# Kernel tuning notes

Measured on AMD Instinct MI355X. Metric: run time of the kernel, lower is better.

## Reference

```python
import jax, jax.numpy as jnp
import numpy as np

D = 512; N = 4096; NH = 16; DEPTH = 3; MLP = 4; GENES = 250; GH = 64; GW = 64


def setup_inputs() -> dict:
    key = jax.random.key(0)
    ks = jax.random.split(key, 10)
    gf = jax.random.normal(ks[0], (N, D), jnp.float32)
    # unique spot positions: permutation of the 64x64 grid cells
    perm = jax.random.permutation(ks[1], GH * GW)[:N]
    coords = jnp.stack([perm // GW, perm % GW], axis=1).astype(jnp.int32)
    s = 0.02
    rn = lambda k, sh: jax.random.normal(k, sh, jnp.float32) * s
    return dict(
        global_feats=gf, coords=coords, grid_h=GH, grid_w=GW,
        ln1_g=jnp.ones((DEPTH, D)), ln1_b=jnp.zeros((DEPTH, D)),
        wqkv=rn(ks[2], (DEPTH, 3 * D, D)), bqkv=jnp.zeros((DEPTH, 3 * D)),
        wo=rn(ks[3], (DEPTH, D, D)), bo=jnp.zeros((DEPTH, D)),
        ln2_g=jnp.ones((DEPTH, D)), ln2_b=jnp.zeros((DEPTH, D)),
        w1=rn(ks[4], (DEPTH, MLP * D, D)), b1=jnp.zeros((DEPTH, MLP * D)),
        w2=rn(ks[5], (DEPTH, D, MLP * D)), b2=jnp.zeros((DEPTH, D)),
        ck=rn(ks[6], (DEPTH, D, 1, 3, 3)), cb=jnp.zeros((DEPTH, D)),
        lnf_g=jnp.ones((D,)), lnf_b=jnp.zeros((D,)),
        wp=rn(ks[7], (GENES, D)), bp=jnp.zeros((GENES,)),
    )


def _ln(x, g, b, eps=1e-5):
    m = jnp.mean(x, axis=-1, keepdims=True)
    v = jnp.var(x, axis=-1, keepdims=True)
    return (x - m) * jax.lax.rsqrt(v + eps) * g + b


def reference(global_feats, coords, grid_h, grid_w, ln1_g, ln1_b, wqkv, bqkv,
              wo, bo, ln2_g, ln2_b, w1, b1, w2, b2, ck, cb, lnf_g, lnf_b, wp, bp):
    x = global_feats  # [N, D]
    n, d = x.shape
    nh = NH; dh = d // nh
    rows = coords[:, 0]; cols = coords[:, 1]
    for i in range(ln1_g.shape[0]):
        # --- self-attention (eval mode, dropout off) ---
        xn = _ln(x, ln1_g[i], ln1_b[i])
        qkv = xn @ wqkv[i].T + bqkv[i]                      # [N, 3D]
        q, k, v = jnp.split(qkv, 3, axis=-1)
        q = q.reshape(n, nh, dh).transpose(1, 0, 2)        # [H, N, dh]
        k = k.reshape(n, nh, dh).transpose(1, 0, 2)
        v = v.reshape(n, nh, dh).transpose(1, 0, 2)
        att = jax.nn.softmax(jnp.einsum('hqd,hkd->hqk', q, k) * (dh ** -0.5), axis=-1)
        ao = jnp.einsum('hqk,hkd->hqd', att, v).transpose(1, 0, 2).reshape(n, d)
        x = x + (ao @ wo[i].T + bo[i])
        # --- MLP ---
        h = jax.nn.gelu(_ln(x, ln2_g[i], ln2_b[i]) @ w1[i].T + b1[i], approximate=False)
        x = x + (h @ w2[i].T + b2[i])
        # --- APEG: scatter -> depthwise conv -> gather ---
        grid = jnp.zeros((d, grid_h, grid_w), x.dtype).at[:, rows, cols].set(x.T)
        co = jax.lax.conv_general_dilated(
            grid[None], ck[i], window_strides=(1, 1), padding=((1, 1), (1, 1)),
            dimension_numbers=('NCHW', 'OIHW', 'NCHW'), feature_group_count=d)[0]
        co = co + cb[i][:, None, None]
        x = x + co[:, rows, cols].T
    x = _ln(x, lnf_g, lnf_b)
    pred = x @ wp.T + bp
    return (x, pred)
```

## Files before the change

kernel.cpp:

```cpp
#include <hip/hip_runtime.h>
#include <math.h>

#define D 512
#define N_TOK 4096
#define NHEAD 16
#define DH 32
#define DEPTH 3
#define MLPD 2048
#define GENES 250
#define GH 64
#define GW 64

typedef __attribute__((ext_vector_type(8))) short short8;
typedef __attribute__((ext_vector_type(4))) float f32x4;
typedef unsigned short ushort_t;

#define AS1 __attribute__((address_space(1)))
#define AS3 __attribute__((address_space(3)))

#if defined(__has_builtin)
#if __has_builtin(__builtin_amdgcn_exp2f)
#define EXP2F(x) __builtin_amdgcn_exp2f(x)
#endif
#endif
#ifndef EXP2F
#define EXP2F(x) __expf(0.69314718056f * (x))
#endif

__device__ __forceinline__ unsigned short f2bf(float f) {
  unsigned int u = __float_as_uint(f);
  u += 0x7fffu + ((u >> 16) & 1u);
  return (unsigned short)(u >> 16);
}
__device__ __forceinline__ unsigned int bfpack(float a, float b) {
  return __builtin_amdgcn_perm(__float_as_uint(b), __float_as_uint(a), 0x07060302u);
}
__device__ __forceinline__ void gload_lds16(const ushort_t* g, ushort_t* l) {
  __builtin_amdgcn_global_load_lds(
      (const AS1 unsigned int*)g,
      (AS3 unsigned int*)(unsigned int)(unsigned long long)l, 16, 0, 0);
}
__device__ __forceinline__ int perm64(int m) {
  int mi = m >> 4, g = (m >> 2) & 3, r = m & 3;
  return ((mi & 1) << 5) | (g << 3) | ((mi >> 1) << 2) | r;
}

__global__ __launch_bounds__(256) void ln_kernel(const float* __restrict__ x,
    const float* __restrict__ g, const float* __restrict__ b,
    float* __restrict__ yf, ushort_t* __restrict__ ybf) {
  int row = blockIdx.x;
  int t = threadIdx.x;
  const float* xr = x + (size_t)row * D;
  float v0 = xr[t], v1 = xr[t + 256];
  float s = v0 + v1;
  float sq = v0 * v0 + v1 * v1;
#pragma unroll
  for (int off = 32; off > 0; off >>= 1) {
    s += __shfl_down(s, off, 64);
    sq += __shfl_down(sq, off, 64);
  }
  __shared__ float s1[4], s2[4];
  int wid = t >> 6, lane = t & 63;
  if (lane == 0) { s1[wid] = s; s2[wid] = sq; }
  __syncthreads();
  float tot = s1[0] + s1[1] + s1[2] + s1[3];
  float totq = s2[0] + s2[1] + s2[2] + s2[3];
  float mean = tot * (1.0f / D);
  float var = totq * (1.0f / D) - mean * mean;
  float rs = rsqrtf(var + 1e-5f);
  float r0 = (v0 - mean) * rs * g[t] + b[t];
  float r1 = (v1 - mean) * rs * g[t + 256] + b[t + 256];
  if (yf) { yf[(size_t)row * D + t] = r0; yf[(size_t)row * D + t + 256] = r1; }
  if (ybf) {
    ybf[(size_t)row * D + t] = f2bf(r0);
    ybf[(size_t)row * D + t + 256] = f2bf(r1);
  }
}

template <int TM, int TN, int NKH>
__global__ __launch_bounds__(256) void gemm_bf(
    const ushort_t* __restrict__ A, const ushort_t* __restrict__ B,
    const float* __restrict__ bias, const float* __restrict__ res,
    float* __restrict__ C, ushort_t* __restrict__ Cbf,
    ushort_t* __restrict__ qO, ushort_t* __restrict__ kO, ushort_t* __restrict__ vO,
    int K, int ldc, int nstore, int mode) {
  constexpr int MI = TM / 32;
  constexpr int NI = TN / 32;
  __shared__ ushort_t As[2][NKH][TM * 32];
  __shared__ ushort_t Bs[2][NKH][TN * 32];
  int t = threadIdx.x;
  int w = t >> 6, lane = t & 63;
  int g = lane >> 4, c = lane & 15;
  int bm = blockIdx.y * TM, bn = blockIdx.x * TN;
  int wr = (w >> 1) * (TM / 2);
  int wc = (w & 1) * (TN / 2);

  const ushort_t* gA = A + (size_t)(bm + (t >> 2)) * K + (t & 3) * 8;
  const ushort_t* gB = B + (size_t)(bn + (t >> 2)) * K + (t & 3) * 8;

  auto stage = [&](int p, int koff) {
#pragma unroll
    for (int h = 0; h < NKH; ++h) {
      gload_lds16(gA + koff + h * 32, &As[p][h][t * 8]);
      if (TM == 128)
        gload_lds16(gA + koff + h * 32 + (size_t)64 * K, &As[p][h][(t + 256) * 8]);
      gload_lds16(gB + koff + h * 32, &Bs[p][h][t * 8]);
      if (TN == 128)
        gload_lds16(gB + koff + h * 32 + (size_t)64 * K, &Bs[p][h][(t + 256) * 8]);
    }
  };

  f32x4 acc[MI][NI] = {};

  const int niter = K / (32 * NKH);
  stage(0, 0);
  __syncthreads();
  for (int it = 0; it < niter; ++it) {
    int p = it & 1;
    if (it + 1 < niter) stage(p ^ 1, (it + 1) * 32 * NKH);
#pragma unroll
    for (int kh = 0; kh < NKH; ++kh) {
      short8 af[MI], bfr[NI];
#pragma unroll
      for (int mi = 0; mi < MI; ++mi)
        af[mi] = *(const short8*)&As[p][kh][(wr + mi * 16 + c) * 32 + g * 8];
#pragma unroll
      for (int ni = 0; ni < NI; ++ni)
        bfr[ni] = *(const short8*)&Bs[p][kh][(wc + ni * 16 + c) * 32 + g * 8];
#pragma unroll
      for (int mi = 0; mi < MI; ++mi)
#pragma unroll
        for (int ni = 0; ni < NI; ++ni)
          acc[mi][ni] = __builtin_amdgcn_mfma_f32_16x16x32_bf16(
              af[mi], bfr[ni], acc[mi][ni], 0, 0, 0);
    }
    __syncthreads();
  }

  const float qs_scale = 0.17677669529663688f * 1.4426950408889634f;
  if (mode == 2) {
#pragma unroll
    for (int ni = 0; ni < NI; ++ni) {
      int col = bn + wc + ni * 16 + c;
      float bv = bias[col];
      int which = col >> 9;
      int h = (col >> 5) & 15;
      int d = col & 31;
      size_t hb = (size_t)h * (N_TOK * DH);
#pragma unroll
      for (int mi = 0; mi < MI; ++mi) {
        int row0 = bm + wr + mi * 16 + g * 4;
        float v0 = acc[mi][ni][0] + bv;
        float v1 = acc[mi][ni][1] + bv;
        float v2 = acc[mi][ni][2] + bv;
        float v3 = acc[mi][ni][3] + bv;
        if (which == 0) {
          qO[hb + (size_t)(row0 + 0) * DH + d] = f2bf(v0 * qs_scale);
          qO[hb + (size_t)(row0 + 1) * DH + d] = f2bf(v1 * qs_scale);
          qO[hb + (size_t)(row0 + 2) * DH + d] = f2bf(v2 * qs_scale);
          qO[hb + (size_t)(row0 + 3) * DH + d] = f2bf(v3 * qs_scale);
        } else if (which == 1) {
          kO[hb + (size_t)(row0 + 0) * DH + d] = f2bf(v0);
          kO[hb + (size_t)(row0 + 1) * DH + d] = f2bf(v1);
          kO[hb + (size_t)(row0 + 2) * DH + d] = f2bf(v2);
          kO[hb + (size_t)(row0 + 3) * DH + d] = f2bf(v3);
        } else {
          int m = row0 & 63;
          int mi_l = m >> 4, g_l = (m >> 2) & 3;
          int nb = ((mi_l & 1) << 5) | (g_l << 3) | ((mi_l >> 1) << 2);
          uint2 pk;
          pk.x = (unsigned)f2bf(v0) | ((unsigned)f2bf(v1) << 16);
          pk.y = (unsigned)f2bf(v2) | ((unsigned)f2bf(v3) << 16);
          *(uint2*)(vO + hb + (size_t)d * N_TOK + (row0 & ~63) + nb) = pk;
        }
      }
    }
    return;
  }
#pragma unroll
  for (int ni = 0; ni < NI; ++ni) {
    int col = bn + wc + ni * 16 + c;
    float bv = bias[col];
    bool cok = col < nstore;
#pragma unroll
    for (int mi = 0; mi < MI; ++mi) {
      int row0 = bm + wr + mi * 16 + g * 4;
#pragma unroll
      for (int reg = 0; reg < 4; ++reg) {
        int row = row0 + reg;
        float v = acc[mi][ni][reg] + bv;
        if (mode == 0) {
          size_t idx = (size_t)row * ldc + col;
          if (cok) {
            if (res) v += res[idx];
            C[idx] = v;
          }
        } else {
          v = 0.5f * v * (1.0f + erff(v * 0.70710678118654752f));
          Cbf[(size_t)row * ldc + col] = f2bf(v);
        }
      }
    }
  }
}

#define VTST 72

__global__ __launch_bounds__(256) void attn_mfma(
    const ushort_t* __restrict__ qb, const ushort_t* __restrict__ kb,
    const ushort_t* __restrict__ vtb, ushort_t* __restrict__ ao) {
  __shared__ ushort_t Vts[2][32 * VTST];
  int qt = blockIdx.x, head = blockIdx.y;
  int t = threadIdx.x;
  int w = t >> 6, lane = t & 63;
  int g = lane >> 4, c = lane & 15;
  const size_t hbase = (size_t)head * (N_TOK * DH);
  int q0 = qt * 128 + w * 32;

  short8 qf[2];
  qf[0] = *(const short8*)(qb + hbase + (size_t)(q0 + c) * DH + g * 8);
  qf[1] = *(const short8*)(qb + hbase + (size_t)(q0 + 16 + c) * DH + g * 8);

  short8 ones;
#pragma unroll
  for (int i = 0; i < 8; ++i) ones[i] = (short)0x3F80;

  f32x4 o[2][2] = {};
  f32x4 lf[2] = {};
  const f32x4 zf = {0.f, 0.f, 0.f, 0.f};

  const ushort_t* vg = vtb + hbase + (size_t)(t >> 3) * N_TOK + (t & 7) * 8;
  const int vofs = (t >> 3) * VTST + (t & 7) * 8;
  const ushort_t* kp = kb + hbase + (size_t)c * DH + g * 8;

  constexpr int NT = N_TOK / 64;
  typedef union { short8 s8; unsigned int u32[4]; } pk_t;

  short8 kfb[2][4];
#pragma unroll
  for (int mi = 0; mi < 4; ++mi)
    kfb[0][mi] = *(const short8*)(kp + (size_t)(mi * 16) * DH);
  {
    short8 v0 = *(const short8*)vg;
    *(short8*)&Vts[0][vofs] = v0;
  }
  short8 vreg = *(const short8*)(vg + 64);
  __syncthreads();

#pragma unroll 2
  for (int tile = 0; tile < NT; ++tile) {
    const int p = tile & 1;
    if (tile + 1 < NT) {
      *(short8*)&Vts[p ^ 1][vofs] = vreg;
      if (tile + 2 < NT) vreg = *(const short8*)(vg + (size_t)(tile + 2) * 64);
#pragma unroll
      for (int mi = 0; mi < 4; ++mi)
        kfb[p ^ 1][mi] =
            *(const short8*)(kp + (size_t)((tile + 1) * 64 + mi * 16) * DH);
    }

    short8 vf[2][2];
#pragma unroll
    for (int half = 0; half < 2; ++half)
#pragma unroll
      for (int ch = 0; ch < 2; ++ch)
        vf[half][ch] = *(const short8*)&Vts[p][(half * 16 + c) * VTST + ch * 32 + g * 8];

    short8 pf[2][2];
#pragma unroll
    for (int qs = 0; qs < 2; ++qs) {
      f32x4 sp[4];
      __builtin_amdgcn_s_setprio(1);
#pragma unroll
      for (int mi = 0; mi < 4; ++mi)
        sp[mi] = __builtin_amdgcn_mfma_f32_16x16x32_bf16(kfb[p][mi], qf[qs], zf, 0, 0, 0);
      __builtin_amdgcn_s_setprio(0);
      float pr[4][4];
#pragma unroll
      for (int mi = 0; mi < 4; ++mi)
#pragma unroll
        for (int r = 0; r < 4; ++r) pr[mi][r] = EXP2F(sp[mi][r]);
      pk_t p0, p1;
      p0.u32[0] = bfpack(pr[0][0], pr[0][1]);
      p0.u32[1] = bfpack(pr[0][2], pr[0][3]);
      p0.u32[2] = bfpack(pr[2][0], pr[2][1]);
      p0.u32[3] = bfpack(pr[2][2], pr[2][3]);
      p1.u32[0] = bfpack(pr[1][0], pr[1][1]);
      p1.u32[1] = bfpack(pr[1][2], pr[1][3]);
      p1.u32[2] = bfpack(pr[3][0], pr[3][1]);
      p1.u32[3] = bfpack(pr[3][2], pr[3][3]);
      pf[qs][0] = p0.s8;
      pf[qs][1] = p1.s8;
    }

    __builtin_amdgcn_s_setprio(1);
#pragma unroll
    for (int qs = 0; qs < 2; ++qs) {
#pragma unroll
      for (int ch = 0; ch < 2; ++ch) {
        lf[qs] = __builtin_amdgcn_mfma_f32_16x16x32_bf16(ones, pf[qs][ch], lf[qs], 0, 0, 0);
#pragma unroll
        for (int half = 0; half < 2; ++half)
          o[qs][half] = __builtin_amdgcn_mfma_f32_16x16x32_bf16(
              vf[half][ch], pf[qs][ch], o[qs][half], 0, 0, 0);
      }
    }
    __builtin_amdgcn_s_setprio(0);
    __syncthreads();
  }

#pragma unroll
  for (int qs = 0; qs < 2; ++qs) {
    float inv = 1.0f / lf[qs][0];
    int q = q0 + qs * 16 + c;
    ushort_t* op = ao + (size_t)q * D + head * DH;
#pragma unroll
    for (int half = 0; half < 2; ++half)
#pragma unroll
      for (int reg = 0; reg < 4; ++reg)
        op[half * 16 + g * 4 + reg] = f2bf(o[qs][half][reg] * inv);
  }
}

__global__ void scatter_kernel(const int* __restrict__ coords,
                               int* __restrict__ pos2tok) {
  int n = blockIdx.x * 256 + threadIdx.x;
  if (n < N_TOK) pos2tok[coords[2 * n] * GW + coords[2 * n + 1]] = n;
}

__global__ __launch_bounds__(256) void conv_ln_kernel(
    const float* __restrict__ xin, float* __restrict__ xout,
    const float* __restrict__ ck, const float* __restrict__ cb,
    const int* __restrict__ pos2tok, const int* __restrict__ coords,
    const float* __restrict__ g, const float* __restrict__ b,
    float* __restrict__ yf, ushort_t* __restrict__ ybf) {
  int n = blockIdx.x, t = threadIdx.x;
  __shared__ int nb[9];
  if (t < 9) {
    int r = coords[2 * n], c = coords[2 * n + 1];
    int dy = t / 3 - 1, dx = t % 3 - 1;
    int rr = r + dy, cc = c + dx;
    nb[t] = (rr >= 0 && rr < GH && cc >= 0 && cc < GW) ? pos2tok[rr * GW + cc] : -1;
  }
  __syncthreads();
  float v[2];
#pragma unroll
  for (int j = 0; j < 2; ++j) {
    int ch = t + j * 256;
    float s = cb[ch];
#pragma unroll
    for (int tap = 0; tap < 9; ++tap) {
      int tok = nb[tap];
      if (tok >= 0) s = fmaf(ck[ch * 9 + tap], xin[(size_t)tok * D + ch], s);
    }
    v[j] = xin[(size_t)n * D + ch] + s;
    xout[(size_t)n * D + ch] = v[j];
  }
  float s = v[0] + v[1];
  float sq = v[0] * v[0] + v[1] * v[1];
#pragma unroll
  for (int off = 32; off > 0; off >>= 1) {
    s += __shfl_down(s, off, 64);
    sq += __shfl_down(sq, off, 64);
  }
  __shared__ float s1[4], s2[4];
  int wid = t >> 6, lane = t & 63;
  if (lane == 0) { s1[wid] = s; s2[wid] = sq; }
  __syncthreads();
  float tot = s1[0] + s1[1] + s1[2] + s1[3];
  float totq = s2[0] + s2[1] + s2[2] + s2[3];
  float mean = tot * (1.0f / D);
  float var = totq * (1.0f / D) - mean * mean;
  float rs = rsqrtf(var + 1e-5f);
  float r0 = (v[0] - mean) * rs * g[t] + b[t];
  float r1 = (v[1] - mean) * rs * g[t + 256] + b[t + 256];
  if (yf) { yf[(size_t)n * D + t] = r0; yf[(size_t)n * D + t + 256] = r1; }
  ybf[(size_t)n * D + t] = f2bf(r0);
  ybf[(size_t)n * D + t + 256] = f2bf(r1);
}

__global__ __launch_bounds__(256) void castw(const float* __restrict__ src,
    ushort_t* __restrict__ dst, int n_src, int n_dst) {
  int i = (blockIdx.x * 256 + threadIdx.x) * 4;
  if (i >= n_dst) return;
  unsigned long long pk = 0;
#pragma unroll
  for (int j = 0; j < 4; ++j) {
    float v = (i + j < n_src) ? src[i + j] : 0.f;
    pk |= ((unsigned long long)f2bf(v)) << (16 * j);
  }
  *(unsigned long long*)(dst + i) = pk;
}

__global__ void pad_bias(const float* __restrict__ src, float* __restrict__ dst) {
  int i = threadIdx.x;
  dst[i] = (i < GENES) ? src[i] : 0.f;
}

extern "C" void kernel_launch(void* const* d_in, const int* in_sizes, int n_in,
                              void* d_out, int out_size, void* d_ws, size_t ws_size,
                              hipStream_t stream) {
  const float* gf     = (const float*)d_in[0];
  const int*   coords = (const int*)d_in[1];
  const float* ln1_g  = (const float*)d_in[4];
  const float* ln1_b  = (const float*)d_in[5];
  const float* wqkv   = (const float*)d_in[6];
  const float* bqkv   = (const float*)d_in[7];
  const float* wo     = (const float*)d_in[8];
  const float* bo     = (const float*)d_in[9];
  const float* ln2_g  = (const float*)d_in[10];
  const float* ln2_b  = (const float*)d_in[11];
  const float* w1     = (const float*)d_in[12];
  const float* b1     = (const float*)d_in[13];
  const float* w2     = (const float*)d_in[14];
  const float* b2     = (const float*)d_in[15];
  const float* ck     = (const float*)d_in[16];
  const float* cb     = (const float*)d_in[17];
  const float* lnf_g  = (const float*)d_in[18];
  const float* lnf_b  = (const float*)d_in[19];
  const float* wp     = (const float*)d_in[20];
  const float* bp     = (const float*)d_in[21];
  float* out = (float*)d_out;

  const size_t ND = (size_t)N_TOK * D;
  float* xb0 = (float*)d_ws;
  float* xb1 = xb0 + ND;
  ushort_t* xn_bf  = (ushort_t*)(xb1 + ND);
  ushort_t* ao_bf  = xn_bf + ND;
  ushort_t* out_bf = ao_bf + ND;
  ushort_t* shared = out_bf + ND;
  ushort_t* qb   = shared;
  ushort_t* kbuf = qb + ND;
  ushort_t* vtb  = kbuf + ND;
  ushort_t* h_bf = shared;
  ushort_t* wqkv_bf = shared + (size_t)N_TOK * MLPD;
  ushort_t* wo_bf = wqkv_bf + DEPTH * 3 * D * D;
  ushort_t* w1_bf = wo_bf + DEPTH * D * D;
  ushort_t* w2_bf = w1_bf + DEPTH * MLPD * D;
  ushort_t* wp_bf = w2_bf + DEPTH * D * MLPD;
  float* bp_pad = (float*)(wp_bf + 256 * D);
  int* pos2tok = (int*)(bp_pad + 256);

  hipMemcpyAsync(xb0, gf, ND * sizeof(float), hipMemcpyDeviceToDevice, stream);
  hipMemsetAsync(pos2tok, 0xFF, GH * GW * sizeof(int), stream);
  scatter_kernel<<<(N_TOK + 255) / 256, 256, 0, stream>>>(coords, pos2tok);

  int nw;
  nw = DEPTH * 3 * D * D;  castw<<<(nw / 4 + 255) / 256, 256, 0, stream>>>(wqkv, wqkv_bf, nw, nw);
  nw = DEPTH * D * D;      castw<<<(nw / 4 + 255) / 256, 256, 0, stream>>>(wo, wo_bf, nw, nw);
  nw = DEPTH * MLPD * D;   castw<<<(nw / 4 + 255) / 256, 256, 0, stream>>>(w1, w1_bf, nw, nw);
  nw = DEPTH * D * MLPD;   castw<<<(nw / 4 + 255) / 256, 256, 0, stream>>>(w2, w2_bf, nw, nw);
  castw<<<(256 * D / 4 + 255) / 256, 256, 0, stream>>>(wp, wp_bf, GENES * D, 256 * D);
  pad_bias<<<1, 256, 0, stream>>>(bp, bp_pad);

  ln_kernel<<<N_TOK, 256, 0, stream>>>(xb0, ln1_g, ln1_b, nullptr, xn_bf);

  float* x  = xb0;
  float* xo = xb1;
  for (int i = 0; i < DEPTH; ++i) {
    gemm_bf<128, 64, 1><<<dim3(24, 32), 256, 0, stream>>>(
        xn_bf, wqkv_bf + (size_t)i * 3 * D * D, bqkv + (size_t)i * 3 * D,
        nullptr, nullptr, nullptr, qb, kbuf, vtb, D, 0, 3 * D, 2);
    attn_mfma<<<dim3(N_TOK / 128, NHEAD), 256, 0, stream>>>(qb, kbuf, vtb, ao_bf);
    gemm_bf<64, 64, 2><<<dim3(8, 64), 256, 0, stream>>>(
        ao_bf, wo_bf + (size_t)i * D * D, bo + (size_t)i * D,
        x, x, nullptr, nullptr, nullptr, nullptr, D, D, D, 0);
    ln_kernel<<<N_TOK, 256, 0, stream>>>(x, ln2_g + i * D, ln2_b + i * D, nullptr, xn_bf);
    gemm_bf<128, 64, 1><<<dim3(32, 32), 256, 0, stream>>>(
        xn_bf, w1_bf + (size_t)i * MLPD * D, b1 + (size_t)i * MLPD,
        nullptr, nullptr, h_bf, nullptr, nullptr, nullptr, D, MLPD, MLPD, 1);
    gemm_bf<64, 64, 2><<<dim3(8, 64), 256, 0, stream>>>(
        h_bf, w2_bf + (size_t)i * D * MLPD, b2 + (size_t)i * D,
        x, x, nullptr, nullptr, nullptr, nullptr, MLPD, D, D, 0);
    if (i < DEPTH - 1) {
      conv_ln_kernel<<<N_TOK, 256, 0, stream>>>(
          x, xo, ck + (size_t)i * D * 9, cb + (size_t)i * D, pos2tok, coords,
          ln1_g + (i + 1) * D, ln1_b + (i + 1) * D, nullptr, xn_bf);
    } else {
      conv_ln_kernel<<<N_TOK, 256, 0, stream>>>(
          x, xo, ck + (size_t)i * D * 9, cb + (size_t)i * D, pos2tok, coords,
          lnf_g, lnf_b, out, out_bf);
    }
    float* tmp = x; x = xo; xo = tmp;
  }
  gemm_bf<64, 64, 2><<<dim3(4, 64), 256, 0, stream>>>(
      out_bf, wp_bf, bp_pad, nullptr, out + ND, nullptr, nullptr, nullptr, nullptr,
      D, GENES, GENES, 0);
}
```

Baseline: 641.9 us.

## Stage K tiles through LDS and software-pipeline QK with PV across tiles

Result: faster. 619.1 us (-3.6%).

```diff
diff --git a/kernel.cpp b/kernel.cpp
--- a/kernel.cpp
+++ b/kernel.cpp
@@ -204,11 +204,13 @@
   }
 }
 
+#define KST 40
 #define VTST 72
 
 __global__ __launch_bounds__(256) void attn_mfma(
     const ushort_t* __restrict__ qb, const ushort_t* __restrict__ kb,
     const ushort_t* __restrict__ vtb, ushort_t* __restrict__ ao) {
+  __shared__ ushort_t Ks[2][64 * KST];
   __shared__ ushort_t Vts[2][32 * VTST];
   int qt = blockIdx.x, head = blockIdx.y;
   int t = threadIdx.x;
@@ -229,57 +231,51 @@
   f32x4 lf[2] = {};
   const f32x4 zf = {0.f, 0.f, 0.f, 0.f};
 
+  const ushort_t* kg = kb + hbase + (size_t)(t >> 2) * DH + (t & 3) * 8;
   const ushort_t* vg = vtb + hbase + (size_t)(t >> 3) * N_TOK + (t & 7) * 8;
+  const int kofs = (t >> 2) * KST + (t & 3) * 8;
   const int vofs = (t >> 3) * VTST + (t & 7) * 8;
-  const ushort_t* kp = kb + hbase + (size_t)c * DH + g * 8;
 
   constexpr int NT = N_TOK / 64;
   typedef union { short8 s8; unsigned int u32[4]; } pk_t;
 
-  short8 kfb[2][4];
-#pragma unroll
-  for (int mi = 0; mi < 4; ++mi)
-    kfb[0][mi] = *(const short8*)(kp + (size_t)(mi * 16) * DH);
+  short8 kreg = *(const short8*)kg;
+  short8 vreg = *(const short8*)vg;
+  *(short8*)&Ks[0][kofs] = kreg;
+  *(short8*)&Vts[0][vofs] = vreg;
+  __syncthreads();
+  kreg = *(const short8*)(kg + (size_t)64 * DH);
+  vreg = *(const short8*)(vg + 64);
+
+  short8 pf_prev[2][2];
+  short8 vf_prev[2][2];
   {
-    short8 v0 = *(const short8*)vg;
-    *(short8*)&Vts[0][vofs] = v0;
-  }
-  short8 vreg = *(const short8*)(vg + 64);
-  __syncthreads();
-
-#pragma unroll 2
-  for (int tile = 0; tile < NT; ++tile) {
-    const int p = tile & 1;
-    if (tile + 1 < NT) {
-      *(short8*)&Vts[p ^ 1][vofs] = vreg;
-      if (tile + 2 < NT) vreg = *(const short8*)(vg + (size_t)(tile + 2) * 64);
+    short8 kf[4];
+#pragma unroll
+    for (int mi = 0; mi < 4; ++mi)
+      kf[mi] = *(const short8*)&Ks[0][(mi * 16 + c) * KST + g * 8];
+#pragma unroll
+    for (int half = 0; half < 2; ++half)
+#pragma unroll
+      for (int ch = 0; ch < 2; ++ch)
+        vf_prev[half][ch] =
+            *(const short8*)&Vts[0][(half * 16 + c) * VTST + ch * 32 + g * 8];
+
+    f32x4 sp[2][4];
+    __builtin_amdgcn_s_setprio(1);
+#pragma unroll
+    for (int qs = 0; qs < 2; ++qs)
 #pragma unroll
       for (int mi = 0; mi < 4; ++mi)
-        kfb[p ^ 1][mi] =
-            *(const short8*)(kp + (size_t)((tile + 1) * 64 + mi * 16) * DH);
-    }
-
-    short8 vf[2][2];
-#pragma unroll
-    for (int half = 0; half < 2; ++half)
-#pragma unroll
-      for (int ch = 0; ch < 2; ++ch)
-        vf[half][ch] = *(const short8*)&Vts[p][(half * 16 + c) * VTST + ch * 32 + g * 8];
-
-    short8 pf[2][2];
+        sp[qs][mi] = __builtin_amdgcn_mfma_f32_16x16x32_bf16(kf[mi], qf[qs], zf, 0, 0, 0);
+    __builtin_amdgcn_s_setprio(0);
 #pragma unroll
     for (int qs = 0; qs < 2; ++qs) {
-      f32x4 sp[4];
-      __builtin_amdgcn_s_setprio(1);
+      float pr[4][4];
 #pragma unroll
       for (int mi = 0; mi < 4; ++mi)
-        sp[mi] = __builtin_amdgcn_mfma_f32_16x16x32_bf16(kfb[p][mi], qf[qs], zf, 0, 0, 0);
-      __builtin_amdgcn_s_setprio(0);
-      float pr[4][4];
-#pragma unroll
-      for (int mi = 0; mi < 4; ++mi)
-#pragma unroll
-        for (int r = 0; r < 4; ++r) pr[mi][r] = EXP2F(sp[mi][r]);
+#pragma unroll
+        for (int r = 0; r < 4; ++r) pr[mi][r] = EXP2F(sp[qs][mi][r]);
       pk_t p0, p1;
       p0.u32[0] = bfpack(pr[0][0], pr[0][1]);
       p0.u32[1] = bfpack(pr[0][2], pr[0][3]);
@@ -289,25 +285,89 @@
       p1.u32[1] = bfpack(pr[1][2], pr[1][3]);
       p1.u32[2] = bfpack(pr[3][0], pr[3][1]);
       p1.u32[3] = bfpack(pr[3][2], pr[3][3]);
-      pf[qs][0] = p0.s8;
-      pf[qs][1] = p1.s8;
-    }
-
+      pf_prev[qs][0] = p0.s8;
+      pf_prev[qs][1] = p1.s8;
+    }
+  }
+
+#pragma unroll 2
+  for (int tile = 1; tile < NT; ++tile) {
+    const int p = tile & 1;
+    *(short8*)&Ks[p][kofs] = kreg;
+    *(short8*)&Vts[p][vofs] = vreg;
+    __syncthreads();
+    if (tile + 1 < NT) {
+      kreg = *(const short8*)(kg + (size_t)(tile + 1) * 64 * DH);
+      vreg = *(const short8*)(vg + (tile + 1) * 64);
+    }
+
+    short8 kf[4], vf[2][2];
+#pragma unroll
+    for (int mi = 0; mi < 4; ++mi)
+      kf[mi] = *(const short8*)&Ks[p][(mi * 16 + c) * KST + g * 8];
+#pragma unroll
+    for (int half = 0; half < 2; ++half)
+#pragma unroll
+      for (int ch = 0; ch < 2; ++ch)
+        vf[half][ch] =
+            *(const short8*)&Vts[p][(half * 16 + c) * VTST + ch * 32 + g * 8];
+
+    f32x4 sp[2][4];
     __builtin_amdgcn_s_setprio(1);
 #pragma unroll
-    for (int qs = 0; qs < 2; ++qs) {
+    for (int qs = 0; qs < 2; ++qs)
+#pragma unroll
+      for (int mi = 0; mi < 4; ++mi)
+        sp[qs][mi] = __builtin_amdgcn_mfma_f32_16x16x32_bf16(kf[mi], qf[qs], zf, 0, 0, 0);
+#pragma unroll
+    for (int qs = 0; qs < 2; ++qs)
 #pragma unroll
       for (int ch = 0; ch < 2; ++ch) {
-        lf[qs] = __builtin_amdgcn_mfma_f32_16x16x32_bf16(ones, pf[qs][ch], lf[qs], 0, 0, 0);
+        lf[qs] = __builtin_amdgcn_mfma_f32_16x16x32_bf16(ones, pf_prev[qs][ch], lf[qs], 0, 0, 0);
 #pragma unroll
         for (int half = 0; half < 2; ++half)
           o[qs][half] = __builtin_amdgcn_mfma_f32_16x16x32_bf16(
-              vf[half][ch], pf[qs][ch], o[qs][half], 0, 0, 0);
+              vf_prev[half][ch], pf_prev[qs][ch], o[qs][half], 0, 0, 0);
       }
-    }
     __builtin_amdgcn_s_setprio(0);
-    __syncthreads();
-  }
+#pragma unroll
+    for (int qs = 0; qs < 2; ++qs) {
+      float pr[4][4];
+#pragma unroll
+      for (int mi = 0; mi < 4; ++mi)
+#pragma unroll
+        for (int r = 0; r < 4; ++r) pr[mi][r] = EXP2F(sp[qs][mi][r]);
+      pk_t p0, p1;
+      p0.u32[0] = bfpack(pr[0][0], pr[0][1]);
+      p0.u32[1] = bfpack(pr[0][2], pr[0][3]);
+      p0.u32[2] = bfpack(pr[2][0], pr[2][1]);
+      p0.u32[3] = bfpack(pr[2][2], pr[2][3]);
+      p1.u32[0] = bfpack(pr[1][0], pr[1][1]);
+      p1.u32[1] = bfpack(pr[1][2], pr[1][3]);
+      p1.u32[2] = bfpack(pr[3][0], pr[3][1]);
+      p1.u32[3] = bfpack(pr[3][2], pr[3][3]);
+      pf_prev[qs][0] = p0.s8;
+      pf_prev[qs][1] = p1.s8;
+    }
+#pragma unroll
+    for (int half = 0; half < 2; ++half)
+#pragma unroll
+      for (int ch = 0; ch < 2; ++ch)
+        vf_prev[half][ch] = vf[half][ch];
+  }
+
+  __builtin_amdgcn_s_setprio(1);
+#pragma unroll
+  for (int qs = 0; qs < 2; ++qs)
+#pragma unroll
+    for (int ch = 0; ch < 2; ++ch) {
+      lf[qs] = __builtin_amdgcn_mfma_f32_16x16x32_bf16(ones, pf_prev[qs][ch], lf[qs], 0, 0, 0);
+#pragma unroll
+      for (int half = 0; half < 2; ++half)
+        o[qs][half] = __builtin_amdgcn_mfma_f32_16x16x32_bf16(
+            vf_prev[half][ch], pf_prev[qs][ch], o[qs][half], 0, 0, 0);
+    }
+  __builtin_amdgcn_s_setprio(0);
 
 #pragma unroll
   for (int qs = 0; qs < 2; ++qs) {
```
